# Kernel tuning notes

Hardware: AMD Instinct MI355X
Metric: run time of the kernel (lower is better)

## Reference

```python
import jax, jax.numpy as jnp
import numpy as np
from jax import lax

D = 1024
H = 1024


def setup_inputs() -> dict:
    key = jax.random.key(0)
    ks = jax.random.split(key, 6)
    N, T = 256, 64
    x = jax.random.normal(ks[0], (N, T, D), dtype=jnp.float32)
    A = jax.random.normal(ks[1], (N, H, 4, 4), dtype=jnp.float32)
    Wx = jax.random.normal(ks[2], (D, 4 * H), dtype=jnp.float32) / np.sqrt(D)
    Wh = jax.random.normal(ks[3], (H, 4 * H), dtype=jnp.float32) / np.sqrt(H)
    Wattn = jax.random.normal(ks[4], (H, 4 * H), dtype=jnp.float32) / np.sqrt(H)
    b = jnp.zeros((4 * H,), dtype=jnp.float32)
    return {"x": x, "A": A, "Wx": Wx, "Wh": Wh, "Wattn": Wattn, "b": b}


def reference(x, A, Wx, Wh, Wattn, b):
    N, T, Din = x.shape
    Hh = A.shape[1]
    A_flat = A.reshape(N, Hh, -1)  # (N, H, 16)
    inv_sqrt_h = jnp.asarray(1.0 / np.sqrt(Hh), dtype=x.dtype)
    h0 = jnp.mean(A, axis=(2, 3))  # (N, H)
    c0 = h0

    def step(carry, xt):
        prev_h, prev_c = carry
        # dot-product attention over the 16 spatial positions
        scores = jnp.einsum('nh,nhp->np', prev_h, A_flat) * inv_sqrt_h
        w = jax.nn.softmax(scores, axis=-1)          # (N, 16)
        attn = jnp.einsum('nhp,np->nh', A_flat, w)   # (N, H)
        # fused LSTM gate preactivation
        a = xt @ Wx + prev_h @ Wh + attn @ Wattn + b  # (N, 4H)
        i, f, o, g = jnp.split(a, 4, axis=-1)
        next_c = jax.nn.sigmoid(f) * prev_c + jax.nn.sigmoid(i) * jnp.tanh(g)
        next_h = jax.nn.sigmoid(o) * jnp.tanh(next_c)
        return (next_h, next_c), next_h

    _, hs = lax.scan(step, (h0, c0), jnp.swapaxes(x, 0, 1))  # hs: (T, N, H)
    return jnp.swapaxes(hs, 0, 1)  # (N, T, H)
```

## Files before the change

### kernel.cpp

```cpp
#include <hip/hip_runtime.h>

typedef __bf16 bf16;
typedef bf16 bf16x8 __attribute__((ext_vector_type(8)));
typedef bf16 bf16x4 __attribute__((ext_vector_type(4)));
typedef float f32x4 __attribute__((ext_vector_type(4)));

#define NB 256
#define TS 64
#define DD 1024
#define HH 1024
#define NOUT 4096


static __device__ __forceinline__ void gload_lds16(const void* g, void* l) {
  __builtin_amdgcn_global_load_lds(
      (const __attribute__((address_space(1))) void*)g,
      (__attribute__((address_space(3))) void*)l, 16, 0, 0);
}

#define SWZ_ADD(v, imm) \
  (v) += __int_as_float(__builtin_amdgcn_ds_swizzle(__float_as_int(v), imm))
#define SWZ_MAX(v, imm) \
  (v) = fmaxf(v, __int_as_float(__builtin_amdgcn_ds_swizzle(__float_as_int(v), imm)))

__global__ __launch_bounds__(256) void convert_x(const float* __restrict__ x,
                                                 bf16* __restrict__ xb) {
  const int gid = blockIdx.x * 256 + threadIdx.x;
  const int t = gid >> 15;
  const int rem = gid & 32767;
  const int n = rem >> 7;
  const int d = (rem & 127) * 8;
  const float* src = x + ((size_t)n * TS + t) * DD + d;
  bf16x8 v;
#pragma unroll
  for (int j = 0; j < 8; ++j) v[j] = (bf16)src[j];
  *(bf16x8*)(xb + (size_t)gid * 8) = v;
}

__global__ __launch_bounds__(1024) void prep_A(const float* __restrict__ A,
                                               bf16* __restrict__ A_bf,
                                               bf16* __restrict__ At,
                                               float* __restrict__ c_ws,
                                               bf16* __restrict__ Aop0,
                                               float* __restrict__ s0) {
  __shared__ float lt[1024 * 17];
  __shared__ float h_sh[1024];
  __shared__ float scA[16], scB[16];
  const int n = (blockIdx.x & 7) * 32 + (blockIdx.x >> 3);
  const int u = threadIdx.x;
  const float* ar = A + ((size_t)n * HH + u) * 16;
  float a[16];
#pragma unroll
  for (int q = 0; q < 4; ++q) {
    const f32x4 v = *(const f32x4*)(ar + q * 4);
#pragma unroll
    for (int r = 0; r < 4; ++r) {
      a[q * 4 + r] = v[r];
      lt[u * 17 + q * 4 + r] = v[r];
    }
  }
  {
    bf16x8 b0, b1;
#pragma unroll
    for (int j = 0; j < 8; ++j) { b0[j] = (bf16)a[j]; b1[j] = (bf16)a[8 + j]; }
    bf16* abf = A_bf + ((size_t)n * HH + u) * 16;
    *(bf16x8*)abf = b0;
    *(bf16x8*)(abf + 8) = b1;
  }
  float h0 = 0.f;
#pragma unroll
  for (int p = 0; p < 16; ++p) h0 += a[p];
  h0 *= 0.0625f;
  c_ws[(n << 10) + u] = h0;
  h_sh[u] = h0;
  Aop0[(n << 10) + u] = (bf16)h0;
  __syncthreads();
  {
    const int p = u >> 6, seg = u & 63;
    bf16x8 o0, o1;
#pragma unroll
    for (int j = 0; j < 8; ++j) {
      o0[j] = (bf16)lt[(seg * 16 + j) * 17 + p];
      o1[j] = (bf16)lt[(seg * 16 + 8 + j) * 17 + p];
    }
    bf16* dst = At + (size_t)(n * 16 + p) * 1024 + seg * 16;
    *(bf16x8*)dst = o0;
    *(bf16x8*)(dst + 8) = o1;
  }
  {
    const int lane = u & 63, w = u >> 6;
    float s = 0.f;
#pragma unroll
    for (int i = 0; i < 16; ++i) {
      const int idx = lane + 64 * i;
      s = fmaf(h_sh[idx], lt[idx * 17 + w], s);
    }
    SWZ_ADD(s, 0x041F); SWZ_ADD(s, 0x081F); SWZ_ADD(s, 0x101F);
    SWZ_ADD(s, 0x201F); SWZ_ADD(s, 0x401F);
    if (lane == 0) scA[w] = s;
    else if (lane == 32) scB[w] = s;
  }
  __syncthreads();
  if (u < 16) s0[n * 16 + u] = scA[u] + scB[u];
}

__global__ __launch_bounds__(256) void convert_wt2(const float* __restrict__ W,
                                                   bf16* __restrict__ Wt) {
  __shared__ bf16 lb[8 * 4096];
  const int kb = blockIdx.x;
  const int kt = kb >> 2, group = kb & 3;
  const int tid = threadIdx.x;
#pragma unroll
  for (int qq = 0; qq < 32; ++qq) {
    const int chunk = qq * 256 + tid;
    const int row = chunk >> 10;
    const int colb = (chunk & 1023) * 4;
    const f32x4 v = *(const f32x4*)(W + (size_t)(kb * 8 + row) * NOUT + colb);
#pragma unroll
    for (int e = 0; e < 4; ++e) {
      const int co = colb + e;
      const int hh = co & 1023, g = co >> 10;
      const int cx = (hh >> 4) * 64 + (hh & 15) * 4 + g;
      lb[row * 4096 + cx] = (bf16)v[e];
    }
  }
  __syncthreads();
  const int tau = tid;
  bf16* wbase = Wt + (size_t)(tau * 32 + kt) * 512 + group * 16 * 8;
#pragma unroll
  for (int c = 0; c < 16; ++c) {
    const int cx = tau * 16 + c;
    bf16x8 o;
#pragma unroll
    for (int j = 0; j < 8; ++j) o[j] = lb[j * 4096 + cx];
    *(bf16x8*)(wbase + c * 8) = o;
  }
}

template <int MODE>
__global__ __launch_bounds__(256, 4) void gemm128(const bf16* __restrict__ Am,
                                                  const bf16* __restrict__ Bt,
                                                  bf16* __restrict__ C,
                                                  const float* __restrict__ bias) {
  __shared__ __align__(16) bf16 astg[2][8 * 512];
  __shared__ __align__(16) bf16 bstg[2][8 * 512];
  const int b = blockIdx.x;
  const int ct = (b & 7) * 4 + ((b >> 3) & 3);
  const int rt = b >> 5;
  const int tid = threadIdx.x, lane = tid & 63, wid = tid >> 6;
  const int wr = wid >> 1, wc = wid & 1;

  const bf16* gA[2];
  const bf16* gB[2];
  int lA[2], lB[2];
#pragma unroll
  for (int e = 0; e < 2; ++e) {
    const int mt = wid * 2 + e;
    gA[e] = Am + (size_t)(rt * 128 + mt * 16 + (lane & 15)) * 1024 + (lane >> 4) * 8;
    lA[e] = mt * 512;
    gB[e] = Bt + ((size_t)(ct * 8 + mt) * 32) * 512 + lane * 8;
    lB[e] = mt * 512;
  }
  f32x4 acc[4][4];
#pragma unroll
  for (int i = 0; i < 4; ++i)
#pragma unroll
    for (int j = 0; j < 4; ++j) acc[i][j] = (f32x4){0, 0, 0, 0};

#pragma unroll
  for (int e = 0; e < 2; ++e) {
    gload_lds16(gA[e], &astg[0][lA[e]]);
    gload_lds16(gB[e], &bstg[0][lB[e]]);
  }
  for (int it = 0; it < 32; ++it) {
    __syncthreads();
    if (it < 31) {
#pragma unroll
      for (int e = 0; e < 2; ++e) {
        gload_lds16(gA[e] + (it + 1) * 32, &astg[(it + 1) & 1][lA[e]]);
        gload_lds16(gB[e] + (size_t)(it + 1) * 512, &bstg[(it + 1) & 1][lB[e]]);
      }
    }
    const bf16* ab = astg[it & 1];
    const bf16* bb = bstg[it & 1];
    bf16x8 af[4], bfr[4];
#pragma unroll
    for (int i = 0; i < 4; ++i) af[i] = *(const bf16x8*)(ab + (wr * 4 + i) * 512 + lane * 8);
#pragma unroll
    for (int j = 0; j < 4; ++j) bfr[j] = *(const bf16x8*)(bb + (wc * 4 + j) * 512 + lane * 8);
#pragma unroll
    for (int i = 0; i < 4; ++i)
#pragma unroll
      for (int j = 0; j < 4; ++j)
        acc[i][j] = __builtin_amdgcn_mfma_f32_16x16x32_bf16(af[i], bfr[j], acc[i][j], 0, 0, 0);
  }
#pragma unroll
  for (int j = 0; j < 4; ++j) {
    const int col = ct * 128 + wc * 64 + j * 16 + (lane & 15);
    float bv = 0.f;
    if (MODE == 0) {
      const int rem = col & 63;
      bv = bias[(rem & 3) * HH + (col >> 6) * 16 + (rem >> 2)];
    }
#pragma unroll
    for (int i = 0; i < 4; ++i) {
      const int row0 = rt * 128 + wr * 64 + i * 16 + (lane >> 4) * 4;
#pragma unroll
      for (int r = 0; r < 4; ++r) {
        const int row = row0 + r;
        size_t idx;
        if (MODE == 0) idx = (size_t)row * NOUT + col;
        else           idx = (size_t)(row >> 4) * (NOUT * 16) + (size_t)col * 16 + (row & 15);
        C[idx] = (bf16)(acc[i][j][r] + bv);
      }
    }
  }
}

#define STEP_SMEM 65536
__global__ __launch_bounds__(512, 4) void step_kernel(
    const bf16* __restrict__ Aop_cur, bf16* __restrict__ Aop_nxt,
    const bf16* __restrict__ Wh_t, const bf16* __restrict__ xWx2,
    const bf16* __restrict__ G2, const float* __restrict__ s_cur,
    float* __restrict__ s_nxt, float* __restrict__ s_zro,
    const bf16* __restrict__ A_bf, float* __restrict__ c_ws,
    float* __restrict__ out, const int t) {
  __shared__ __align__(16) char smem[STEP_SMEM];
  __shared__ float w_sh[512];
  bf16* astg = (bf16*)smem;
  float* red = (float*)smem;

  const int b = blockIdx.x;
  const int xcd = b & 7;
  const int ht = xcd * 8 + ((b >> 3) & 7);
  const int rt = b >> 6;
  const int tid = threadIdx.x, lane = tid & 63, wid = tid >> 6;
  const int kg = wid >> 1, ow = wid & 1;
  const int nloc = tid >> 4, hl = tid & 15;
  const int n = rt * 32 + nloc, h = ht * 16 + hl;

  float ss = s_cur[n * 16 + hl];

#pragma unroll
  for (int e = 0; e < 8; ++e) {
    const int tau = wid * 8 + e;
    const int tkg = tau >> 4, tmt = (tau >> 3) & 1, tks = tau & 7;
    const bf16* src = Aop_cur +
        (size_t)(rt * 32 + tmt * 16 + (lane & 15)) * 1024 +
        tkg * 256 + tks * 32 + (lane >> 4) * 8;
    gload_lds16(src, astg + tkg * 8192 + (tmt * 8 + tks) * 512);
  }

  bf16x8 gq[8];
  {
    const bf16* Gp = G2 + (size_t)n * (NOUT * 16) + (size_t)(ht * 64 + hl * 4) * 16;
#pragma unroll
    for (int e = 0; e < 8; ++e) gq[e] = *(const bf16x8*)(Gp + e * 8);
  }
  const bf16x4 xv = *(const bf16x4*)(xWx2 + (size_t)t * (NB * NOUT) +
                                     (size_t)n * NOUT + ht * 64 + hl * 4);
  if (tid < 8) s_zro[b * 8 + tid] = 0.f;

  {
    ss *= 0.03125f;
    float m = ss;
    SWZ_MAX(m, 0x041F); SWZ_MAX(m, 0x081F); SWZ_MAX(m, 0x101F); SWZ_MAX(m, 0x201F);
    const float e = expf(ss - m);
    float su = e;
    SWZ_ADD(su, 0x041F); SWZ_ADD(su, 0x081F); SWZ_ADD(su, 0x101F); SWZ_ADD(su, 0x201F);
    w_sh[tid] = e / su;
  }
  __syncthreads();

  const bf16* gB0 = Wh_t + ((size_t)(ht * 4 + ow * 2 + 0) * 32 + kg * 8) * 512 + lane * 8;
  const bf16* gB1 = Wh_t + ((size_t)(ht * 4 + ow * 2 + 1) * 32 + kg * 8) * 512 + lane * 8;
  f32x4 a00 = {0, 0, 0, 0}, a01 = {0, 0, 0, 0}, a10 = {0, 0, 0, 0}, a11 = {0, 0, 0, 0};
  {
    const bf16* ab = astg + kg * 8192;
    bf16x8 bc0 = *(const bf16x8*)gB0;
    bf16x8 bc1 = *(const bf16x8*)gB1;
    __builtin_amdgcn_s_setprio(1);
#pragma unroll
    for (int ks = 0; ks < 8; ++ks) {
      bf16x8 bn0, bn1;
      if (ks < 7) {
        bn0 = *(const bf16x8*)(gB0 + (ks + 1) * 512);
        bn1 = *(const bf16x8*)(gB1 + (ks + 1) * 512);
      }
      const bf16x8 f0 = *(const bf16x8*)(ab + ks * 512 + lane * 8);
      const bf16x8 f1 = *(const bf16x8*)(ab + (8 + ks) * 512 + lane * 8);
      a00 = __builtin_amdgcn_mfma_f32_16x16x32_bf16(f0, bc0, a00, 0, 0, 0);
      a01 = __builtin_amdgcn_mfma_f32_16x16x32_bf16(f0, bc1, a01, 0, 0, 0);
      a10 = __builtin_amdgcn_mfma_f32_16x16x32_bf16(f1, bc0, a10, 0, 0, 0);
      a11 = __builtin_amdgcn_mfma_f32_16x16x32_bf16(f1, bc1, a11, 0, 0, 0);
      if (ks < 7) { bc0 = bn0; bc1 = bn1; }
    }
    __builtin_amdgcn_s_setprio(0);
  }
  __syncthreads();

  {
    const int cb = kg * 64 + ow * 32 + (lane & 15);
    const int nb = (lane >> 4) * 4;
    *(f32x4*)&red[(cb)*36 + nb] = a00;
    *(f32x4*)&red[(cb + 16) * 36 + nb] = a01;
    *(f32x4*)&red[(cb)*36 + nb + 16] = a10;
    *(f32x4*)&red[(cb + 16) * 36 + nb + 16] = a11;
  }
  __syncthreads();

  f32x4 gv = {0, 0, 0, 0};
#pragma unroll
  for (int k2 = 0; k2 < 4; ++k2)
#pragma unroll
    for (int g = 0; g < 4; ++g) gv[g] += red[(k2 * 64 + hl * 4 + g) * 36 + nloc];
#pragma unroll
  for (int g = 0; g < 4; ++g) {
    float a0 = 0.f;
#pragma unroll
    for (int p = 0; p < 8; ++p) a0 = fmaf(w_sh[nloc * 16 + p], (float)gq[g * 2][p], a0);
#pragma unroll
    for (int p = 0; p < 8; ++p) a0 = fmaf(w_sh[nloc * 16 + 8 + p], (float)gq[g * 2 + 1][p], a0);
    gv[g] += a0;
  }
  const float ai = gv[0] + (float)xv[0];
  const float af = gv[1] + (float)xv[1];
  const float ao = gv[2] + (float)xv[2];
  const float ag = gv[3] + (float)xv[3];
  const float cold = c_ws[(n << 10) + h];
  const float si = 1.f / (1.f + expf(-ai));
  const float sf = 1.f / (1.f + expf(-af));
  const float so = 1.f / (1.f + expf(-ao));
  const float cn = sf * cold + si * tanhf(ag);
  const float hn = so * tanhf(cn);
  c_ws[(n << 10) + h] = cn;
  out[((size_t)n * TS + t) * HH + h] = hn;
  Aop_nxt[(n << 10) + h] = (bf16)hn;

  if (t < TS - 1) {
    __syncthreads();
    const bf16* arow = A_bf + ((size_t)n * HH + h) * 16;
    const bf16x8 av0 = *(const bf16x8*)arow;
    const bf16x8 av1 = *(const bf16x8*)(arow + 8);
#pragma unroll
    for (int r = 0; r < 8; ++r) {
      red[(nloc * 16 + r) * 17 + hl] = hn * (float)av0[r];
      red[(nloc * 16 + 8 + r) * 17 + hl] = hn * (float)av1[r];
    }
    __syncthreads();
    const float* r2 = &red[(nloc * 16 + hl) * 17];
    float s = 0.f;
#pragma unroll
    for (int q = 0; q < 16; ++q) s += r2[q];
    atomicAdd(&s_nxt[n * 16 + hl], s);
  }
}

extern "C" void kernel_launch(void* const* d_in, const int* in_sizes, int n_in,
                              void* d_out, int out_size, void* d_ws, size_t ws_size,
                              hipStream_t stream) {
  const float* x     = (const float*)d_in[0];
  const float* A     = (const float*)d_in[1];
  const float* Wx    = (const float*)d_in[2];
  const float* Wh    = (const float*)d_in[3];
  const float* Wattn = (const float*)d_in[4];
  const float* bias  = (const float*)d_in[5];
  float* out = (float*)d_out;
  char* ws = (char*)d_ws;
  bf16* Wh_t   = (bf16*)(ws + 0);
  bf16* Wat_t  = (bf16*)(ws + 8388608);
  bf16* At     = (bf16*)(ws + 16777216);
  bf16* A_bf   = (bf16*)(ws + 25165824);
  bf16* xWx2   = (bf16*)(ws + 33554432);
  bf16* G2     = (bf16*)(ws + 167772160);
  bf16* x_bf   = (bf16*)(ws + 201326592);
  bf16* Wxt    = (bf16*)(ws + 234881024);
  bf16* Aop0   = (bf16*)(ws + 243269632);
  bf16* Aop1   = (bf16*)(ws + 243793920);
  float* s0    = (float*)(ws + 244318208);
  float* s1    = (float*)(ws + 244334592);
  float* s2    = (float*)(ws + 244350976);
  float* c_ws  = (float*)(ws + 244367360);

  hipMemsetAsync(s1, 0, 16384, stream);
  convert_x<<<8192, 256, 0, stream>>>(x, x_bf);
  prep_A<<<256, 1024, 0, stream>>>(A, A_bf, At, c_ws, Aop0, s0);
  convert_wt2<<<128, 256, 0, stream>>>(Wx, Wxt);
  convert_wt2<<<128, 256, 0, stream>>>(Wh, Wh_t);
  convert_wt2<<<128, 256, 0, stream>>>(Wattn, Wat_t);
  gemm128<0><<<4096, 256, 0, stream>>>(x_bf, Wxt, xWx2, bias);
  gemm128<1><<<1024, 256, 0, stream>>>(At, Wat_t, G2, nullptr);
  for (int t = 0; t < TS; ++t) {
    float* scur = (t % 3 == 0) ? s0 : (t % 3 == 1) ? s1 : s2;
    float* snxt = (t % 3 == 0) ? s1 : (t % 3 == 1) ? s2 : s0;
    float* szro = (t % 3 == 0) ? s2 : (t % 3 == 1) ? s0 : s1;
    step_kernel<<<512, 512, 0, stream>>>((t & 1) ? Aop1 : Aop0,
                                         (t & 1) ? Aop0 : Aop1, Wh_t, xWx2,
                                         G2, scur, snxt, szro, A_bf, c_ws,
                                         out, t);
  }
}
```

Before: 1.399 ms.

## Load recurrent A operand directly into registers instead of staging through LDS

The per-step kernel stops staging the previous hidden-state tile into LDS via global_load_lds and instead loads each wave's MFMA A fragments straight into registers. This removes a __syncthreads, shrinks shared memory from 64KB to 36KB, and hoists the c and first Wh loads earlier. The G2 attention loads move after the MFMA loop, and the output store becomes nontemporal. The cost is higher register pressure (16 extra bf16x8 per thread) and redundant global reads of A fragments across waves, since the two ow waves of each kg load the same data.

```diff
diff --git a/kernel.cpp b/kernel.cpp
--- a/kernel.cpp
+++ b/kernel.cpp
@@ -217,7 +217,7 @@
   }
 }
 
-#define STEP_SMEM 65536
+#define STEP_SMEM 36864
 __global__ __launch_bounds__(512, 4) void step_kernel(
     const bf16* __restrict__ Aop_cur, bf16* __restrict__ Aop_nxt,
     const bf16* __restrict__ Wh_t, const bf16* __restrict__ xWx2,
@@ -225,10 +225,8 @@
     float* __restrict__ s_nxt, float* __restrict__ s_zro,
     const bf16* __restrict__ A_bf, float* __restrict__ c_ws,
     float* __restrict__ out, const int t) {
-  __shared__ __align__(16) char smem[STEP_SMEM];
+  __shared__ __align__(16) float red[9216];
   __shared__ float w_sh[512];
-  bf16* astg = (bf16*)smem;
-  float* red = (float*)smem;
 
   const int b = blockIdx.x;
   const int xcd = b & 7;
@@ -241,24 +239,23 @@
 
   float ss = s_cur[n * 16 + hl];
 
-#pragma unroll
-  for (int e = 0; e < 8; ++e) {
-    const int tau = wid * 8 + e;
-    const int tkg = tau >> 4, tmt = (tau >> 3) & 1, tks = tau & 7;
-    const bf16* src = Aop_cur +
-        (size_t)(rt * 32 + tmt * 16 + (lane & 15)) * 1024 +
-        tkg * 256 + tks * 32 + (lane >> 4) * 8;
-    gload_lds16(src, astg + tkg * 8192 + (tmt * 8 + tks) * 512);
-  }
-
-  bf16x8 gq[8];
-  {
-    const bf16* Gp = G2 + (size_t)n * (NOUT * 16) + (size_t)(ht * 64 + hl * 4) * 16;
-#pragma unroll
-    for (int e = 0; e < 8; ++e) gq[e] = *(const bf16x8*)(Gp + e * 8);
-  }
+  const bf16* aBase0 = Aop_cur + (size_t)(rt * 32 + (lane & 15)) * 1024 +
+                       kg * 256 + (lane >> 4) * 8;
+  const bf16* aBase1 = aBase0 + 16 * 1024;
+  bf16x8 af0[8], af1[8];
+#pragma unroll
+  for (int ks = 0; ks < 8; ++ks) {
+    af0[ks] = *(const bf16x8*)(aBase0 + ks * 32);
+    af1[ks] = *(const bf16x8*)(aBase1 + ks * 32);
+  }
+
   const bf16x4 xv = *(const bf16x4*)(xWx2 + (size_t)t * (NB * NOUT) +
                                      (size_t)n * NOUT + ht * 64 + hl * 4);
+  const float cold = c_ws[(n << 10) + h];
+  const bf16* gB0 = Wh_t + ((size_t)(ht * 4 + ow * 2 + 0) * 32 + kg * 8) * 512 + lane * 8;
+  const bf16* gB1 = Wh_t + ((size_t)(ht * 4 + ow * 2 + 1) * 32 + kg * 8) * 512 + lane * 8;
+  bf16x8 bc0 = *(const bf16x8*)gB0;
+  bf16x8 bc1 = *(const bf16x8*)gB1;
   if (tid < 8) s_zro[b * 8 + tid] = 0.f;
 
   {
@@ -270,15 +267,9 @@
     SWZ_ADD(su, 0x041F); SWZ_ADD(su, 0x081F); SWZ_ADD(su, 0x101F); SWZ_ADD(su, 0x201F);
     w_sh[tid] = e / su;
   }
-  __syncthreads();
-
-  const bf16* gB0 = Wh_t + ((size_t)(ht * 4 + ow * 2 + 0) * 32 + kg * 8) * 512 + lane * 8;
-  const bf16* gB1 = Wh_t + ((size_t)(ht * 4 + ow * 2 + 1) * 32 + kg * 8) * 512 + lane * 8;
+
   f32x4 a00 = {0, 0, 0, 0}, a01 = {0, 0, 0, 0}, a10 = {0, 0, 0, 0}, a11 = {0, 0, 0, 0};
   {
-    const bf16* ab = astg + kg * 8192;
-    bf16x8 bc0 = *(const bf16x8*)gB0;
-    bf16x8 bc1 = *(const bf16x8*)gB1;
     __builtin_amdgcn_s_setprio(1);
 #pragma unroll
     for (int ks = 0; ks < 8; ++ks) {
@@ -287,17 +278,21 @@
         bn0 = *(const bf16x8*)(gB0 + (ks + 1) * 512);
         bn1 = *(const bf16x8*)(gB1 + (ks + 1) * 512);
       }
-      const bf16x8 f0 = *(const bf16x8*)(ab + ks * 512 + lane * 8);
-      const bf16x8 f1 = *(const bf16x8*)(ab + (8 + ks) * 512 + lane * 8);
-      a00 = __builtin_amdgcn_mfma_f32_16x16x32_bf16(f0, bc0, a00, 0, 0, 0);
-      a01 = __builtin_amdgcn_mfma_f32_16x16x32_bf16(f0, bc1, a01, 0, 0, 0);
-      a10 = __builtin_amdgcn_mfma_f32_16x16x32_bf16(f1, bc0, a10, 0, 0, 0);
-      a11 = __builtin_amdgcn_mfma_f32_16x16x32_bf16(f1, bc1, a11, 0, 0, 0);
+      a00 = __builtin_amdgcn_mfma_f32_16x16x32_bf16(af0[ks], bc0, a00, 0, 0, 0);
+      a01 = __builtin_amdgcn_mfma_f32_16x16x32_bf16(af0[ks], bc1, a01, 0, 0, 0);
+      a10 = __builtin_amdgcn_mfma_f32_16x16x32_bf16(af1[ks], bc0, a10, 0, 0, 0);
+      a11 = __builtin_amdgcn_mfma_f32_16x16x32_bf16(af1[ks], bc1, a11, 0, 0, 0);
       if (ks < 7) { bc0 = bn0; bc1 = bn1; }
     }
     __builtin_amdgcn_s_setprio(0);
   }
-  __syncthreads();
+
+  bf16x8 gq[8];
+  {
+    const bf16* Gp = G2 + (size_t)n * (NOUT * 16) + (size_t)(ht * 64 + hl * 4) * 16;
+#pragma unroll
+    for (int e = 0; e < 8; ++e) gq[e] = *(const bf16x8*)(Gp + e * 8);
+  }
 
   {
     const int cb = kg * 64 + ow * 32 + (lane & 15);
@@ -327,14 +322,13 @@
   const float af = gv[1] + (float)xv[1];
   const float ao = gv[2] + (float)xv[2];
   const float ag = gv[3] + (float)xv[3];
-  const float cold = c_ws[(n << 10) + h];
   const float si = 1.f / (1.f + expf(-ai));
   const float sf = 1.f / (1.f + expf(-af));
   const float so = 1.f / (1.f + expf(-ao));
   const float cn = sf * cold + si * tanhf(ag);
   const float hn = so * tanhf(cn);
   c_ws[(n << 10) + h] = cn;
-  out[((size_t)n * TS + t) * HH + h] = hn;
+  __builtin_nontemporal_store(hn, &out[((size_t)n * TS + t) * HH + h]);
   Aop_nxt[(n << 10) + h] = (bf16)hn;
 
   if (t < TS - 1) {
```

Result: slower. 1.487 ms (+6.3%).
